# Kernel tuning notes

Measured on AMD Instinct MI355X. Metric: run time of the kernel, lower is better.

Reference implementation:

```python
import jax, jax.numpy as jnp
import numpy as np

N_SR = 50000; N_TG = 50000; DIM = 256; VAL_DIM = 300; ATT_NUM = 1001
N_VAL = 100000; E_ATTR = 200000; E_EDGE = 400000; N_SEED = 10000


def _build_adj(rng, n, e):
    # replicate preprocess_adj: symmetrize, add self-loops, coalesce + clamp(values,1)
    edges = rng.integers(0, n, size=(e, 2))
    und = np.concatenate([edges, edges[:, ::-1]], axis=0)
    loops = np.repeat(np.arange(n)[:, None], 2, axis=1)
    uniq = np.unique(np.concatenate([und, loops], axis=0), axis=0)  # coalesced binary adj
    return jnp.asarray(uniq[:, 0], jnp.int32), jnp.asarray(uniq[:, 1], jnp.int32)


def _xavier(k, shape):
    fan_in, fan_out = shape[0], shape[-1]
    s = jnp.sqrt(6.0 / (fan_in + fan_out)).astype(jnp.float32)
    return jax.random.uniform(k, shape, jnp.float32, -1.0, 1.0) * s


def setup_inputs():
    rng = np.random.default_rng(0)
    ks = jax.random.split(jax.random.key(0), 10)

    def triples(n_ent):
        return jnp.asarray(np.stack([rng.integers(0, n_ent, E_ATTR),
                                     rng.integers(0, N_VAL, E_ATTR),
                                     rng.integers(0, ATT_NUM, E_ATTR)], axis=1), jnp.int32)

    r_sr, c_sr = _build_adj(rng, N_SR, E_EDGE)
    r_tg, c_tg = _build_adj(rng, N_TG, E_EDGE)
    return {
        'ent_seed_sr': jnp.asarray(rng.integers(0, N_SR, N_SEED), jnp.int32),
        'ent_seed_tg': jnp.asarray(rng.integers(0, N_TG, N_SEED), jnp.int32),
        'attribute_triples_sr': triples(N_SR),
        'attribute_triples_tg': triples(N_TG),
        'adj_rows_sr': r_sr, 'adj_cols_sr': c_sr,
        'adj_rows_tg': r_tg, 'adj_cols_tg': c_tg,
        'att_feats': _xavier(ks[0], (ATT_NUM, DIM)),
        'val_feats': jax.random.normal(ks[1], (N_VAL, VAL_DIM), jnp.float32),
        'ent_feats_sr': _xavier(ks[2], (N_SR, DIM)),
        'ent_feats_tg': _xavier(ks[3], (N_TG, DIM)),
        'a_w': _xavier(ks[4], (2 * DIM, 1)).reshape(-1),
        'a_b': jnp.zeros((1,), jnp.float32),
        'W_enc': _xavier(ks[5], (DIM + VAL_DIM, DIM)),
        'gcn_w1': _xavier(ks[6], (DIM, DIM)),
        'gcn_b1': jnp.zeros((DIM,), jnp.float32),
        'gcn_w2': _xavier(ks[7], (DIM, DIM)),
        'gcn_b2': jnp.zeros((DIM,), jnp.float32),
    }


def attributed_encoder(triples, att_feats, val_feats, ent_feats, a_w, a_b, W_enc):
    h, val, att = triples[:, 0], triples[:, 1], triples[:, 2]
    n = ent_feats.shape[0]
    # edge attention score: Linear(cat(ent[h], att[att])) -> exp(leaky_relu(.))
    score = jnp.concatenate([ent_feats[h], att_feats[att]], axis=-1) @ a_w + a_b[0]  # [E]
    score = jnp.exp(jax.nn.leaky_relu(score, negative_slope=0.2))
    row_sum = jax.ops.segment_sum(score, h, num_segments=n)      # sparse softmax denom
    p = score / row_sum[h]                                       # [E]
    av = jnp.concatenate([att_feats[att], val_feats[val]], axis=-1) @ W_enc  # [E, DIM]
    agg = jax.ops.segment_sum(av * p[:, None], h, num_segments=n)
    return jax.nn.elu(agg + ent_feats)


def gcn_layer(rows, cols, feats, w, b, act):
    n = feats.shape[0]
    agg = jax.ops.segment_sum(feats[cols], rows, num_segments=n)           # A @ feats
    deg = jax.ops.segment_sum(jnp.ones(rows.shape, feats.dtype), rows, num_segments=n)
    h = act((agg / deg[:, None]) @ w + b)
    return feats + h  # residual, dims match


def _l2norm(x):
    return x / jnp.maximum(jnp.linalg.norm(x, axis=-1, keepdims=True), 1e-12)


def reference(ent_seed_sr, ent_seed_tg, attribute_triples_sr, attribute_triples_tg,
              adj_rows_sr, adj_cols_sr, adj_rows_tg, adj_cols_tg,
              att_feats, val_feats, ent_feats_sr, ent_feats_tg,
              a_w, a_b, W_enc, gcn_w1, gcn_b1, gcn_w2, gcn_b2):
    fs = attributed_encoder(attribute_triples_sr, att_feats, val_feats, ent_feats_sr, a_w, a_b, W_enc)
    ft = attributed_encoder(attribute_triples_tg, att_feats, val_feats, ent_feats_tg, a_w, a_b, W_enc)
    fs = gcn_layer(adj_rows_sr, adj_cols_sr, fs, gcn_w1, gcn_b1, jax.nn.relu)
    ft = gcn_layer(adj_rows_tg, adj_cols_tg, ft, gcn_w1, gcn_b1, jax.nn.relu)
    fs = gcn_layer(adj_rows_sr, adj_cols_sr, fs, gcn_w2, gcn_b2, lambda x: x)
    ft = gcn_layer(adj_rows_tg, adj_cols_tg, ft, gcn_w2, gcn_b2, lambda x: x)
    fs = _l2norm(fs)
    ft = _l2norm(ft)
    return fs[ent_seed_sr], ft[ent_seed_tg], fs, ft
```

## Files before the change

### kernel.cpp

```cpp
#include <hip/hip_runtime.h>
#include <math.h>

#define DIM 256
#define VAL_DIM 300

typedef __attribute__((ext_vector_type(8))) short short8;
typedef __attribute__((ext_vector_type(4))) float fx4;

__device__ __forceinline__ short f2bf(float x) {
    unsigned u = __float_as_uint(x);
    unsigned r = (u + 0x7fff + ((u >> 16) & 1)) >> 16;
    return (short)r;
}
__device__ __forceinline__ float bf2f(short h) {
    return __uint_as_float(((unsigned)(unsigned short)h) << 16);
}

__global__ void k_split_b(const float* __restrict__ W, short* __restrict__ Bhi,
                          short* __restrict__ Blo, int Kreal, int Kp, int Ncols) {
    int idx = blockIdx.x * 256 + threadIdx.x;
    int total = (Ncols / 16) * (Kp / 32) * 64;
    if (idx >= total) return;
    int lane = idx & 63;
    int kt = (idx >> 6) % (Kp / 32);
    int nt = (idx >> 6) / (Kp / 32);
    int n = nt * 16 + (lane & 15);
    int kbase = kt * 32 + ((lane >> 4) & 3) * 8;
    short h[8], l[8];
#pragma unroll
    for (int j = 0; j < 8; ++j) {
        int k = kbase + j;
        float x = (k < Kreal) ? W[(size_t)k * Ncols + n] : 0.f;
        short hh = f2bf(x);
        float r = x - bf2f(hh);
        h[j] = hh;
        l[j] = f2bf(r);
    }
    size_t base = (size_t)idx * 8;
#pragma unroll
    for (int j = 0; j < 8; ++j) { Bhi[base + j] = h[j]; Blo[base + j] = l[j]; }
}

template <int MODE>
__global__ void k_gemm(const float* __restrict__ A, const short* __restrict__ Bhi,
                       const short* __restrict__ Blo, const float* __restrict__ bias,
                       float* __restrict__ Out, int M, int K, int Kp) {
    __shared__ short Ah[8 * 512];
    __shared__ short Al[8 * 512];
    const int m0 = blockIdx.x * 64;
    const int tid = threadIdx.x;
    const int wave = tid >> 6;
    const int lane = tid & 63;
    const int wm = wave >> 2;
    const int wn = wave & 3;
    fx4 acc[2][4] = {};

    for (int pk = 0; pk < Kp; pk += 64) {
        {
            int ss = tid;
            int mt = ss >> 7;
            int ks = (ss >> 6) & 1;
            int ln = ss & 63;
            int row = m0 + mt * 16 + (ln & 15);
            int kk = pk + ks * 32 + ((ln >> 4) & 3) * 8;
            float v[8];
            if (row < M && kk + 8 <= K) {
                fx4 u0 = *(const fx4*)&A[(size_t)row * K + kk];
                fx4 u1 = *(const fx4*)&A[(size_t)row * K + kk + 4];
                v[0] = u0[0]; v[1] = u0[1]; v[2] = u0[2]; v[3] = u0[3];
                v[4] = u1[0]; v[5] = u1[1]; v[6] = u1[2]; v[7] = u1[3];
            } else {
#pragma unroll
                for (int j = 0; j < 8; ++j)
                    v[j] = (row < M && kk + j < K) ? A[(size_t)row * K + kk + j] : 0.f;
            }
            short8 h8, l8;
#pragma unroll
            for (int j = 0; j < 8; ++j) {
                short hh = f2bf(v[j]);
                h8[j] = hh;
                l8[j] = f2bf(v[j] - bf2f(hh));
            }
            *(short8*)&Ah[(mt * 2 + ks) * 512 + ln * 8] = h8;
            *(short8*)&Al[(mt * 2 + ks) * 512 + ln * 8] = l8;
        }
        __syncthreads();
#pragma unroll
        for (int ks = 0; ks < 2; ++ks) {
            int kglob = pk + ks * 32;
            short8 ah[2], al[2], bh[4], bl[4];
#pragma unroll
            for (int t = 0; t < 2; ++t) {
                ah[t] = *(short8*)&Ah[((wm * 2 + t) * 2 + ks) * 512 + lane * 8];
                al[t] = *(short8*)&Al[((wm * 2 + t) * 2 + ks) * 512 + lane * 8];
            }
#pragma unroll
            for (int t = 0; t < 4; ++t) {
                int ntg = wn * 4 + t;
                size_t fb = ((size_t)(ntg * (Kp >> 5) + (kglob >> 5))) * 512 + lane * 8;
                bh[t] = *(const short8*)&Bhi[fb];
                bl[t] = *(const short8*)&Blo[fb];
            }
#pragma unroll
            for (int i = 0; i < 2; ++i)
#pragma unroll
                for (int j = 0; j < 4; ++j) {
                    acc[i][j] = __builtin_amdgcn_mfma_f32_16x16x32_bf16(ah[i], bh[j], acc[i][j], 0, 0, 0);
                    acc[i][j] = __builtin_amdgcn_mfma_f32_16x16x32_bf16(ah[i], bl[j], acc[i][j], 0, 0, 0);
                    acc[i][j] = __builtin_amdgcn_mfma_f32_16x16x32_bf16(al[i], bh[j], acc[i][j], 0, 0, 0);
                }
        }
        __syncthreads();
    }
    const int quad = lane >> 4;
    const int cl = lane & 15;
#pragma unroll
    for (int i = 0; i < 2; ++i) {
        int rbase = m0 + (wm * 2 + i) * 16 + quad * 4;
#pragma unroll
        for (int j = 0; j < 4; ++j) {
            int col = (wn * 4 + j) * 16 + cl;
            float bb = (MODE == 0) ? 0.f : bias[col];
#pragma unroll
            for (int r = 0; r < 4; ++r) {
                int row = rbase + r;
                if (row >= M) continue;
                if (MODE == 0) {
                    Out[(size_t)row * DIM + col] = acc[i][j][r];
                } else {
                    float h = acc[i][j][r] + bb;
                    if (MODE == 1) h = fmaxf(h, 0.f);
                    Out[(size_t)row * DIM + col] += h;
                }
            }
        }
    }
}

__global__ void k_att(const float* __restrict__ att_feats, const float* __restrict__ W_enc,
                      const float* __restrict__ a_w, float* __restrict__ att_proj,
                      float* __restrict__ att_score) {
    int a = blockIdx.x;
    int j = threadIdx.x;
    __shared__ float row[DIM];
    __shared__ float red[DIM];
    float v = att_feats[a * DIM + j];
    row[j] = v;
    red[j] = v * a_w[DIM + j];
    __syncthreads();
    for (int s = 128; s > 0; s >>= 1) {
        if (j < s) red[j] += red[j + s];
        __syncthreads();
    }
    if (j == 0) att_score[a] = red[0];
    float acc = 0.f;
    for (int d = 0; d < DIM; ++d)
        acc += row[d] * W_enc[d * DIM + j];
    att_proj[a * DIM + j] = acc;
}

__global__ void k_ent_score(const float* __restrict__ ent, const float* __restrict__ a_w,
                            float* __restrict__ score) {
    int i = blockIdx.x;
    int j = threadIdx.x;
    __shared__ float red[DIM];
    red[j] = ent[(size_t)i * DIM + j] * a_w[j];
    __syncthreads();
    for (int s = 128; s > 0; s >>= 1) {
        if (j < s) red[j] += red[j + s];
        __syncthreads();
    }
    if (j == 0) score[i] = red[0];
}

__global__ void k_edge_score(const int* __restrict__ triples, const float* __restrict__ ent_score,
                             const float* __restrict__ att_score, const float* __restrict__ a_b,
                             float* __restrict__ edge_w, float* __restrict__ row_sum,
                             int* __restrict__ cnt, int* __restrict__ rank, int e_attr) {
    int e = blockIdx.x * blockDim.x + threadIdx.x;
    if (e >= e_attr) return;
    int h = triples[e * 3 + 0];
    int att = triples[e * 3 + 2];
    float s = ent_score[h] + att_score[att] + a_b[0];
    s = (s >= 0.f) ? s : 0.2f * s;
    float w = expf(s);
    edge_w[e] = w;
    atomicAdd(&row_sum[h], w);
    rank[e] = atomicAdd(&cnt[h], 1);
}

__global__ void k_blocksum(const int* __restrict__ cnt, int* __restrict__ bsum, int n) {
    int i = blockIdx.x * 256 + threadIdx.x;
    int v = (i < n) ? cnt[i] : 0;
    __shared__ int red[256];
    red[threadIdx.x] = v;
    __syncthreads();
    for (int s = 128; s > 0; s >>= 1) {
        if (threadIdx.x < s) red[threadIdx.x] += red[threadIdx.x + s];
        __syncthreads();
    }
    if (threadIdx.x == 0) bsum[blockIdx.x] = red[0];
}

__global__ void k_scan_bsum(int* __restrict__ bsum, int nb) {
    int t = threadIdx.x;
    int v = (t < nb) ? bsum[t] : 0;
    __shared__ int buf[256];
    buf[t] = v;
    __syncthreads();
    for (int s = 1; s < 256; s <<= 1) {
        int tv = (t >= s) ? buf[t - s] : 0;
        __syncthreads();
        buf[t] += tv;
        __syncthreads();
    }
    if (t < nb) bsum[t] = buf[t] - v;
}

__global__ void k_scan_final(const int* __restrict__ cnt, const int* __restrict__ bsum,
                             int* __restrict__ off, int n) {
    int b = blockIdx.x;
    int t = threadIdx.x;
    int i = b * 256 + t;
    int v = (i < n) ? cnt[i] : 0;
    __shared__ int buf[256];
    buf[t] = v;
    __syncthreads();
    for (int s = 1; s < 256; s <<= 1) {
        int tv = (t >= s) ? buf[t - s] : 0;
        __syncthreads();
        buf[t] += tv;
        __syncthreads();
    }
    if (i < n) off[i] = bsum[b] + buf[t] - v;
    if (i == n - 1) off[n] = bsum[b] + buf[t];
}

__global__ void k_scatter(const int* __restrict__ triples, const int* __restrict__ rank,
                          const int* __restrict__ off, int* __restrict__ eidx, int e_attr) {
    int e = blockIdx.x * blockDim.x + threadIdx.x;
    if (e >= e_attr) return;
    int h = triples[e * 3 + 0];
    eidx[off[h] + rank[e]] = e;
}

__global__ void k_edge_agg_csr(const int* __restrict__ triples, const float* __restrict__ edge_w,
                               const float* __restrict__ row_sum, const int* __restrict__ off,
                               const int* __restrict__ eidx, const fx4* __restrict__ att_proj,
                               const fx4* __restrict__ val_proj, const fx4* __restrict__ ent,
                               fx4* __restrict__ F, int n) {
    int wave = threadIdx.x >> 6;
    int lane = threadIdx.x & 63;
    int h = blockIdx.x * 4 + wave;
    if (h >= n) return;
    int s = off[h], e = off[h + 1];
    fx4 acc = {};
    float inv = (e > s) ? 1.0f / row_sum[h] : 0.f;
    for (int j = s; j < e; ++j) {
        int ed = eidx[j];
        int val = triples[ed * 3 + 1];
        int att = triples[ed * 3 + 2];
        float p = edge_w[ed] * inv;
        acc += p * (att_proj[(size_t)att * 64 + lane] + val_proj[(size_t)val * 64 + lane]);
    }
    fx4 x = acc + ent[(size_t)h * 64 + lane];
    fx4 r;
#pragma unroll
    for (int c = 0; c < 4; ++c) r[c] = (x[c] > 0.f) ? x[c] : expm1f(x[c]);
    F[(size_t)h * 64 + lane] = r;
}

__global__ void k_deg(const int* __restrict__ rows, int n_edges, int n,
                      int* __restrict__ off, float* __restrict__ deg_inv) {
    int i = blockIdx.x * blockDim.x + threadIdx.x;
    if (i > n) return;
    int lo = 0, hi = n_edges;
    while (lo < hi) {
        int m = (lo + hi) >> 1;
        if (rows[m] < i) lo = m + 1; else hi = m;
    }
    off[i] = lo;
    if (i < n) {
        int lo2 = lo, hi2 = n_edges;
        while (lo2 < hi2) {
            int m = (lo2 + hi2) >> 1;
            if (rows[m] < i + 1) lo2 = m + 1; else hi2 = m;
        }
        int d = lo2 - lo;
        deg_inv[i] = 1.0f / (float)(d > 0 ? d : 1);
    }
}

__global__ void k_gcn_agg(const int* __restrict__ off, const int* __restrict__ cols,
                          const float* __restrict__ deg_inv, const fx4* __restrict__ F,
                          fx4* __restrict__ T, int n) {
    int wave = threadIdx.x >> 6;
    int lane = threadIdx.x & 63;
    int i = blockIdx.x * 4 + wave;
    if (i >= n) return;
    int s = off[i], e = off[i + 1];
    fx4 acc = {};
    for (int k = s; k < e; ++k) {
        int c = cols[k];
        acc += F[(size_t)c * 64 + lane];
    }
    T[(size_t)i * 64 + lane] = acc * deg_inv[i];
}

__global__ void k_norm_out(const float* __restrict__ F, float* __restrict__ out) {
    int i = blockIdx.x;
    int j = threadIdx.x;
    __shared__ float red[DIM];
    float v = F[(size_t)i * DIM + j];
    red[j] = v * v;
    __syncthreads();
    for (int s = 128; s > 0; s >>= 1) {
        if (j < s) red[j] += red[j + s];
        __syncthreads();
    }
    float sc = 1.0f / fmaxf(sqrtf(red[0]), 1e-12f);
    out[(size_t)i * DIM + j] = v * sc;
}

__global__ void k_gather(const int* __restrict__ seed, const float* __restrict__ full,
                         float* __restrict__ out) {
    int i = blockIdx.x;
    int j = threadIdx.x;
    out[(size_t)i * DIM + j] = full[(size_t)seed[i] * DIM + j];
}

extern "C" void kernel_launch(void* const* d_in, const int* in_sizes, int n_in,
                              void* d_out, int out_size, void* d_ws, size_t ws_size,
                              hipStream_t stream) {
    const int* seed_sr = (const int*)d_in[0];
    const int* seed_tg = (const int*)d_in[1];
    const int* tri_sr = (const int*)d_in[2];
    const int* tri_tg = (const int*)d_in[3];
    const int* rows_sr = (const int*)d_in[4];
    const int* cols_sr = (const int*)d_in[5];
    const int* rows_tg = (const int*)d_in[6];
    const int* cols_tg = (const int*)d_in[7];
    const float* att_feats = (const float*)d_in[8];
    const float* val_feats = (const float*)d_in[9];
    const float* ent_sr = (const float*)d_in[10];
    const float* ent_tg = (const float*)d_in[11];
    const float* a_w = (const float*)d_in[12];
    const float* a_b = (const float*)d_in[13];
    const float* W_enc = (const float*)d_in[14];
    const float* w1 = (const float*)d_in[15];
    const float* b1 = (const float*)d_in[16];
    const float* w2 = (const float*)d_in[17];
    const float* b2 = (const float*)d_in[18];

    const int N = in_sizes[10] / DIM;
    const int n_att = in_sizes[8] / DIM;
    const int n_val = in_sizes[9] / VAL_DIM;
    const int e_attr = in_sizes[2] / 3;
    const int n_seed = in_sizes[0];
    const int KpV = 320;
    const int nb = (N + 255) / 256;

    char* p = (char*)d_ws;
    auto alloc = [&](size_t nbytes) -> void* {
        void* r = (void*)p;
        p += (nbytes + 255) & ~(size_t)255;
        return r;
    };
    float* val_proj = (float*)alloc(sizeof(float) * (size_t)n_val * DIM);
    float* att_proj = (float*)alloc(sizeof(float) * (size_t)n_att * DIM);
    float* att_score = (float*)alloc(sizeof(float) * (size_t)n_att);
    float* ent_score = (float*)alloc(sizeof(float) * (size_t)N);
    float* row_sum = (float*)alloc(sizeof(float) * (size_t)N);
    float* edge_w = (float*)alloc(sizeof(float) * (size_t)e_attr);
    float* deg_inv = (float*)alloc(sizeof(float) * (size_t)N);
    int* off = (int*)alloc(sizeof(int) * (size_t)(N + 1));
    int* off_csr = (int*)alloc(sizeof(int) * (size_t)(N + 1));
    int* cnt = (int*)alloc(sizeof(int) * (size_t)N);
    int* rank = (int*)alloc(sizeof(int) * (size_t)e_attr);
    int* bsum = (int*)alloc(sizeof(int) * (size_t)nb);
    int* eidx = (int*)alloc(sizeof(int) * (size_t)e_attr);
    float* F = (float*)alloc(sizeof(float) * (size_t)N * DIM);
    float* T = (float*)alloc(sizeof(float) * (size_t)N * DIM);
    short* wencv_hi = (short*)alloc(sizeof(short) * (DIM / 16) * (KpV / 32) * 512);
    short* wencv_lo = (short*)alloc(sizeof(short) * (DIM / 16) * (KpV / 32) * 512);
    short* w1_hi = (short*)alloc(sizeof(short) * (DIM / 16) * (DIM / 32) * 512);
    short* w1_lo = (short*)alloc(sizeof(short) * (DIM / 16) * (DIM / 32) * 512);
    short* w2_hi = (short*)alloc(sizeof(short) * (DIM / 16) * (DIM / 32) * 512);
    short* w2_lo = (short*)alloc(sizeof(short) * (DIM / 16) * (DIM / 32) * 512);

    float* out = (float*)d_out;
    float* out_seed_arr[2] = { out, out + (size_t)n_seed * DIM };
    float* out_full_arr[2] = { out + (size_t)2 * n_seed * DIM,
                               out + (size_t)2 * n_seed * DIM + (size_t)N * DIM };

    {
        int tot_v = (DIM / 16) * (KpV / 32) * 64;
        k_split_b<<<(tot_v + 255) / 256, 256, 0, stream>>>(W_enc + (size_t)DIM * DIM, wencv_hi,
                                                           wencv_lo, VAL_DIM, KpV, DIM);
        int tot_w = (DIM / 16) * (DIM / 32) * 64;
        k_split_b<<<(tot_w + 255) / 256, 256, 0, stream>>>(w1, w1_hi, w1_lo, DIM, DIM, DIM);
        k_split_b<<<(tot_w + 255) / 256, 256, 0, stream>>>(w2, w2_hi, w2_lo, DIM, DIM, DIM);
    }

    k_att<<<n_att, DIM, 0, stream>>>(att_feats, W_enc, a_w, att_proj, att_score);
    k_gemm<0><<<(n_val + 63) / 64, 512, 0, stream>>>(val_feats, wencv_hi, wencv_lo, nullptr,
                                                     val_proj, n_val, VAL_DIM, KpV);

    const int* tris[2] = { tri_sr, tri_tg };
    const float* ents[2] = { ent_sr, ent_tg };
    const int* rws[2] = { rows_sr, rows_tg };
    const int* cls[2] = { cols_sr, cols_tg };
    const int eadj[2] = { in_sizes[4], in_sizes[6] };
    const int* seeds[2] = { seed_sr, seed_tg };

    for (int s = 0; s < 2; ++s) {
        k_ent_score<<<N, DIM, 0, stream>>>(ents[s], a_w, ent_score);
        hipMemsetAsync(row_sum, 0, sizeof(float) * (size_t)N, stream);
        hipMemsetAsync(cnt, 0, sizeof(int) * (size_t)N, stream);
        k_edge_score<<<(e_attr + 255) / 256, 256, 0, stream>>>(tris[s], ent_score, att_score,
                                                               a_b, edge_w, row_sum, cnt, rank,
                                                               e_attr);
        k_blocksum<<<nb, 256, 0, stream>>>(cnt, bsum, N);
        k_scan_bsum<<<1, 256, 0, stream>>>(bsum, nb);
        k_scan_final<<<nb, 256, 0, stream>>>(cnt, bsum, off_csr, N);
        k_scatter<<<(e_attr + 255) / 256, 256, 0, stream>>>(tris[s], rank, off_csr, eidx, e_attr);
        k_edge_agg_csr<<<(N + 3) / 4, 256, 0, stream>>>(tris[s], edge_w, row_sum, off_csr, eidx,
                                                        (const fx4*)att_proj, (const fx4*)val_proj,
                                                        (const fx4*)ents[s], (fx4*)F, N);
        k_deg<<<(N + 1 + 255) / 256, 256, 0, stream>>>(rws[s], eadj[s], N, off, deg_inv);
        k_gcn_agg<<<(N + 3) / 4, 256, 0, stream>>>(off, cls[s], deg_inv, (const fx4*)F, (fx4*)T, N);
        k_gemm<1><<<(N + 63) / 64, 512, 0, stream>>>(T, w1_hi, w1_lo, b1, F, N, DIM, DIM);
        k_gcn_agg<<<(N + 3) / 4, 256, 0, stream>>>(off, cls[s], deg_inv, (const fx4*)F, (fx4*)T, N);
        k_gemm<2><<<(N + 63) / 64, 512, 0, stream>>>(T, w2_hi, w2_lo, b2, F, N, DIM, DIM);
        k_norm_out<<<N, DIM, 0, stream>>>(F, out_full_arr[s]);
        k_gather<<<n_seed, DIM, 0, stream>>>(seeds[s], out_full_arr[s], out_seed_arr[s]);
    }
}
```

Baseline: 1.420 ms.

## Store val_proj and gather features in fp16 to halve gather traffic

The value-projection output is written as fp16, and fp16 shadow copies of the entity features are emitted next to the fp32 ones. The attribute aggregation and both GCN neighbour aggregations now gather the fp16 rows, halving the bytes moved in these random-access gathers. The GCN gather loop is also unrolled by four so more loads are in flight at once. The trade-off is extra fp16 writes and reduced precision in the aggregated sums, which could affect output tolerance.

Result: faster. 1.174 ms (-17.3%).

```diff
diff --git a/kernel.cpp b/kernel.cpp
--- a/kernel.cpp
+++ b/kernel.cpp
@@ -6,6 +6,8 @@
 
 typedef __attribute__((ext_vector_type(8))) short short8;
 typedef __attribute__((ext_vector_type(4))) float fx4;
+typedef _Float16 f16;
+typedef __attribute__((ext_vector_type(4))) _Float16 h4;
 
 __device__ __forceinline__ short f2bf(float x) {
     unsigned u = __float_as_uint(x);
@@ -44,7 +46,7 @@
 template <int MODE>
 __global__ void k_gemm(const float* __restrict__ A, const short* __restrict__ Bhi,
                        const short* __restrict__ Blo, const float* __restrict__ bias,
-                       float* __restrict__ Out, int M, int K, int Kp) {
+                       float* __restrict__ Out, f16* __restrict__ Out16, int M, int K, int Kp) {
     __shared__ short Ah[8 * 512];
     __shared__ short Al[8 * 512];
     const int m0 = blockIdx.x * 64;
@@ -125,12 +127,16 @@
             for (int r = 0; r < 4; ++r) {
                 int row = rbase + r;
                 if (row >= M) continue;
+                size_t idx = (size_t)row * DIM + col;
                 if (MODE == 0) {
-                    Out[(size_t)row * DIM + col] = acc[i][j][r];
+                    Out16[idx] = (f16)acc[i][j][r];
+                } else if (MODE == 1) {
+                    float h = fmaxf(acc[i][j][r] + bb, 0.f);
+                    float v = Out[idx] + h;
+                    Out[idx] = v;
+                    Out16[idx] = (f16)v;
                 } else {
-                    float h = acc[i][j][r] + bb;
-                    if (MODE == 1) h = fmaxf(h, 0.f);
-                    Out[(size_t)row * DIM + col] += h;
+                    Out[idx] += acc[i][j][r] + bb;
                 }
             }
         }
@@ -247,8 +253,8 @@
 __global__ void k_edge_agg_csr(const int* __restrict__ triples, const float* __restrict__ edge_w,
                                const float* __restrict__ row_sum, const int* __restrict__ off,
                                const int* __restrict__ eidx, const fx4* __restrict__ att_proj,
-                               const fx4* __restrict__ val_proj, const fx4* __restrict__ ent,
-                               fx4* __restrict__ F, int n) {
+                               const h4* __restrict__ val_proj, const fx4* __restrict__ ent,
+                               fx4* __restrict__ F, h4* __restrict__ F16, int n) {
     int wave = threadIdx.x >> 6;
     int lane = threadIdx.x & 63;
     int h = blockIdx.x * 4 + wave;
@@ -261,13 +267,21 @@
         int val = triples[ed * 3 + 1];
         int att = triples[ed * 3 + 2];
         float p = edge_w[ed] * inv;
-        acc += p * (att_proj[(size_t)att * 64 + lane] + val_proj[(size_t)val * 64 + lane]);
+        fx4 a = att_proj[(size_t)att * 64 + lane];
+        h4 v = val_proj[(size_t)val * 64 + lane];
+#pragma unroll
+        for (int c = 0; c < 4; ++c) acc[c] += p * (a[c] + (float)v[c]);
     }
     fx4 x = acc + ent[(size_t)h * 64 + lane];
     fx4 r;
-#pragma unroll
-    for (int c = 0; c < 4; ++c) r[c] = (x[c] > 0.f) ? x[c] : expm1f(x[c]);
+    h4 r16;
+#pragma unroll
+    for (int c = 0; c < 4; ++c) {
+        r[c] = (x[c] > 0.f) ? x[c] : expm1f(x[c]);
+        r16[c] = (f16)r[c];
+    }
     F[(size_t)h * 64 + lane] = r;
+    F16[(size_t)h * 64 + lane] = r16;
 }
 
 __global__ void k_deg(const int* __restrict__ rows, int n_edges, int n,
@@ -292,7 +306,7 @@
 }
 
 __global__ void k_gcn_agg(const int* __restrict__ off, const int* __restrict__ cols,
-                          const float* __restrict__ deg_inv, const fx4* __restrict__ F,
+                          const float* __restrict__ deg_inv, const h4* __restrict__ F16,
                           fx4* __restrict__ T, int n) {
     int wave = threadIdx.x >> 6;
     int lane = threadIdx.x & 63;
@@ -300,9 +314,21 @@
     if (i >= n) return;
     int s = off[i], e = off[i + 1];
     fx4 acc = {};
-    for (int k = s; k < e; ++k) {
-        int c = cols[k];
-        acc += F[(size_t)c * 64 + lane];
+    int k = s;
+    for (; k + 4 <= e; k += 4) {
+        int c0 = cols[k], c1 = cols[k + 1], c2 = cols[k + 2], c3 = cols[k + 3];
+        h4 r0 = F16[(size_t)c0 * 64 + lane];
+        h4 r1 = F16[(size_t)c1 * 64 + lane];
+        h4 r2 = F16[(size_t)c2 * 64 + lane];
+        h4 r3 = F16[(size_t)c3 * 64 + lane];
+#pragma unroll
+        for (int c = 0; c < 4; ++c)
+            acc[c] += ((float)r0[c] + (float)r1[c]) + ((float)r2[c] + (float)r3[c]);
+    }
+    for (; k < e; ++k) {
+        h4 r = F16[(size_t)cols[k] * 64 + lane];
+#pragma unroll
+        for (int c = 0; c < 4; ++c) acc[c] += (float)r[c];
     }
     T[(size_t)i * 64 + lane] = acc * deg_inv[i];
 }
@@ -366,7 +392,7 @@
         p += (nbytes + 255) & ~(size_t)255;
         return r;
     };
-    float* val_proj = (float*)alloc(sizeof(float) * (size_t)n_val * DIM);
+    f16* val16 = (f16*)alloc(sizeof(f16) * (size_t)n_val * DIM);
     float* att_proj = (float*)alloc(sizeof(float) * (size_t)n_att * DIM);
     float* att_score = (float*)alloc(sizeof(float) * (size_t)n_att);
     float* ent_score = (float*)alloc(sizeof(float) * (size_t)N);
@@ -380,6 +406,7 @@
     int* bsum = (int*)alloc(sizeof(int) * (size_t)nb);
     int* eidx = (int*)alloc(sizeof(int) * (size_t)e_attr);
     float* F = (float*)alloc(sizeof(float) * (size_t)N * DIM);
+    f16* F16 = (f16*)alloc(sizeof(f16) * (size_t)N * DIM);
     float* T = (float*)alloc(sizeof(float) * (size_t)N * DIM);
     short* wencv_hi = (short*)alloc(sizeof(short) * (DIM / 16) * (KpV / 32) * 512);
     short* wencv_lo = (short*)alloc(sizeof(short) * (DIM / 16) * (KpV / 32) * 512);
@@ -404,7 +431,7 @@
 
     k_att<<<n_att, DIM, 0, stream>>>(att_feats, W_enc, a_w, att_proj, att_score);
     k_gemm<0><<<(n_val + 63) / 64, 512, 0, stream>>>(val_feats, wencv_hi, wencv_lo, nullptr,
-                                                     val_proj, n_val, VAL_DIM, KpV);
+                                                     nullptr, val16, n_val, VAL_DIM, KpV);
 
     const int* tris[2] = { tri_sr, tri_tg };
     const float* ents[2] = { ent_sr, ent_tg };
@@ -425,13 +452,13 @@
         k_scan_final<<<nb, 256, 0, stream>>>(cnt, bsum, off_csr, N);
         k_scatter<<<(e_attr + 255) / 256, 256, 0, stream>>>(tris[s], rank, off_csr, eidx, e_attr);
         k_edge_agg_csr<<<(N + 3) / 4, 256, 0, stream>>>(tris[s], edge_w, row_sum, off_csr, eidx,
-                                                        (const fx4*)att_proj, (const fx4*)val_proj,
-                                                        (const fx4*)ents[s], (fx4*)F, N);
+                                                        (const fx4*)att_proj, (const h4*)val16,
+                                                        (const fx4*)ents[s], (fx4*)F, (h4*)F16, N);
         k_deg<<<(N + 1 + 255) / 256, 256, 0, stream>>>(rws[s], eadj[s], N, off, deg_inv);
-        k_gcn_agg<<<(N + 3) / 4, 256, 0, stream>>>(off, cls[s], deg_inv, (const fx4*)F, (fx4*)T, N);
-        k_gemm<1><<<(N + 63) / 64, 512, 0, stream>>>(T, w1_hi, w1_lo, b1, F, N, DIM, DIM);
-        k_gcn_agg<<<(N + 3) / 4, 256, 0, stream>>>(off, cls[s], deg_inv, (const fx4*)F, (fx4*)T, N);
-        k_gemm<2><<<(N + 63) / 64, 512, 0, stream>>>(T, w2_hi, w2_lo, b2, F, N, DIM, DIM);
+        k_gcn_agg<<<(N + 3) / 4, 256, 0, stream>>>(off, cls[s], deg_inv, (const h4*)F16, (fx4*)T, N);
+        k_gemm<1><<<(N + 63) / 64, 512, 0, stream>>>(T, w1_hi, w1_lo, b1, F, F16, N, DIM, DIM);
+        k_gcn_agg<<<(N + 3) / 4, 256, 0, stream>>>(off, cls[s], deg_inv, (const h4*)F16, (fx4*)T, N);
+        k_gemm<2><<<(N + 63) / 64, 512, 0, stream>>>(T, w2_hi, w2_lo, b2, F, nullptr, N, DIM, DIM);
         k_norm_out<<<N, DIM, 0, stream>>>(F, out_full_arr[s]);
         k_gather<<<n_seed, DIM, 0, stream>>>(seeds[s], out_full_arr[s], out_seed_arr[s]);
     }
```
